# Kernel optimization log

Hardware: AMD Instinct MI355X
Metric: run time of the kernel (lower is better)

## Reference

```python
import jax, jax.numpy as jnp
import numpy as np

B, S, D = 2, 2048, 1024
H, HD = 16, 64


def setup_inputs() -> dict:
    key = jax.random.key(0)
    ks = jax.random.split(key, 10)
    scale = 1.0 / np.sqrt(D)
    inputs_q = jax.random.normal(ks[0], (B, S, D), dtype=jnp.float32)
    inputs_kv = jax.random.normal(ks[1], (B, S, D), dtype=jnp.float32)
    # causal mask, broadcast over batch: True = attend
    mask = jnp.broadcast_to(jnp.tril(jnp.ones((S, S), dtype=bool)), (B, S, S))
    Wq = jax.random.normal(ks[2], (D, H * HD), dtype=jnp.float32) * scale
    bq = jnp.zeros((H * HD,), dtype=jnp.float32)
    Wk = jax.random.normal(ks[3], (D, H * HD), dtype=jnp.float32) * scale
    bk = jnp.zeros((H * HD,), dtype=jnp.float32)
    Wv = jax.random.normal(ks[4], (D, H * HD), dtype=jnp.float32) * scale
    bv = jnp.zeros((H * HD,), dtype=jnp.float32)
    Wo = jax.random.normal(ks[5], (H * HD, D), dtype=jnp.float32) * scale
    bo = jnp.zeros((D,), dtype=jnp.float32)
    return {"inputs_q": inputs_q, "inputs_kv": inputs_kv, "mask": mask,
            "Wq": Wq, "bq": bq, "Wk": Wk, "bk": bk, "Wv": Wv, "bv": bv,
            "Wo": Wo, "bo": bo}


def reference(inputs_q, inputs_kv, mask, Wq, bq, Wk, bk, Wv, bv, Wo, bo):
    b, s_q, _ = inputs_q.shape
    s_k = inputs_kv.shape[1]
    # projections -> [B, S, H, HD]
    q = (inputs_q @ Wq + bq).reshape(b, s_q, H, HD)
    k = (inputs_kv @ Wk + bk).reshape(b, s_k, H, HD)
    v = (inputs_kv @ Wv + bv).reshape(b, s_k, H, HD)
    q = q / jnp.sqrt(jnp.asarray(HD, dtype=q.dtype))
    # scores: [B, H, Sq, Sk]
    attn = jnp.einsum('bqhd,bkhd->bhqk', q, k)
    m = mask[:, None, :, :]  # [B,1,Sq,Sk] broadcast over heads
    attn = jnp.where(m, attn, jnp.asarray(-1e30, dtype=attn.dtype))
    attn = jax.nn.softmax(attn, axis=-1)
    # dropout_rate = 0.0, deterministic -> identity
    out = jnp.einsum('bhqk,bkhd->bqhd', attn, v).reshape(b, s_q, H * HD)
    return out @ Wo + bo
```

## Files before the change

### kernel.cpp

```cpp
#include <hip/hip_runtime.h>

typedef __attribute__((ext_vector_type(4))) float f32x4;
typedef __attribute__((ext_vector_type(8))) short bf16x8;
typedef unsigned short u16;
typedef unsigned int u32;

#define AS1 __attribute__((address_space(1)))
#define AS3 __attribute__((address_space(3)))

#define WAITVM(N) do{ asm volatile("s_waitcnt vmcnt(" #N ")" ::: "memory"); \
                      __builtin_amdgcn_sched_barrier(0); }while(0)
#define RAWBAR    do{ __builtin_amdgcn_s_barrier();                          \
                      __builtin_amdgcn_sched_barrier(0); }while(0)

__device__ __forceinline__ float fast_exp2(float x){
  return __builtin_amdgcn_exp2f(x);
}

__device__ __forceinline__ u16 f2bf(float x){
  u32 u = __float_as_uint(x);
  u += 0x7fffu + ((u >> 16) & 1u);
  return (u16)(u >> 16);
}
__device__ __forceinline__ u16 f2bf_fast(float x){
  return (u16)((__float_as_uint(x) + 0x8000u) >> 16);
}

__global__ __launch_bounds__(256) void prep(const float* __restrict__ W0,
                                            const float* __restrict__ W1,
                                            const float* __restrict__ W2,
                                            const float* __restrict__ W3,
                                            u16* __restrict__ Wt,
                                            const float* __restrict__ inq,
                                            const float* __restrict__ inkv,
                                            u16* __restrict__ Xq,
                                            u16* __restrict__ Xkv)
{
  const int z = blockIdx.z;
  if (z < 4){
    __shared__ float tile[32][33];
    const float* src = z == 0 ? W0 : z == 1 ? W1 : z == 2 ? W2 : W3;
    u16* d = Wt + (size_t)z * 1024 * 1024;
    int tx = threadIdx.x & 31, ty = threadIdx.x >> 5;
    int k0 = blockIdx.x * 32, n0 = blockIdx.y * 32;
    for (int r = 0; r < 4; ++r)
      tile[ty + r * 8][tx] = src[(size_t)(k0 + ty + r * 8) * 1024 + n0 + tx];
    __syncthreads();
    for (int r = 0; r < 4; ++r)
      d[(size_t)(n0 + ty + r * 8) * 1024 + k0 + tx] = f2bf(tile[tx][ty + r * 8]);
  } else {
    const float* src = z == 4 ? inq : inkv;
    u16* dst = z == 4 ? Xq : Xkv;
    int bid = blockIdx.y * 32 + blockIdx.x;
    size_t base4 = ((size_t)bid * 256 + threadIdx.x) * 4;
#pragma unroll
    for (int i = 0; i < 4; ++i){
      float4 v = reinterpret_cast<const float4*>(src)[base4 + i];
      ushort4 o;
      o.x = f2bf(v.x); o.y = f2bf(v.y); o.z = f2bf(v.z); o.w = f2bf(v.w);
      reinterpret_cast<ushort4*>(dst)[base4 + i] = o;
    }
  }
}

__global__ __launch_bounds__(512, 2) void gemm_qkv(const u16* __restrict__ Xq,
                                                   const u16* __restrict__ Xkv,
                                                   const u16* __restrict__ Wt,
                                                   const float* __restrict__ bq,
                                                   const float* __restrict__ bk,
                                                   const float* __restrict__ bv,
                                                   u16* __restrict__ Qb,
                                                   u16* __restrict__ Kb,
                                                   u16* __restrict__ Vt,
                                                   int M, int K)
{
  __shared__ u16 lA[3][256 * 32];
  __shared__ u16 lB[3][256 * 32];
  const int tid = threadIdx.x;
  const int l = tid & 63, w = tid >> 6;
  const int wr = w >> 2, wc = w & 3;
  const int bm0 = blockIdx.x * 256, bn0 = blockIdx.y * 256;
  const int seg = bn0 >> 10;
  const int nloc0 = bn0 & 1023;
  const u16* A = seg ? Xkv : Xq;
  const float* bias = seg == 0 ? bq : seg == 1 ? bk : bv;
  const float scale = seg == 0 ? 0.125f * 1.44269504089f : 1.0f;
  const int lr = l & 15, g4 = l >> 4;

#define STAGE_A(BI, KK) do{                                                   \
  _Pragma("unroll") for (int c_ = 0; c_ < 2; ++c_){                           \
    int e_ = c_ * 512 + tid;                                                  \
    int row_ = e_ >> 2, ch_ = e_ & 3;                                         \
    int sc_ = (ch_ ^ (row_ & 3)) * 8;                                         \
    __builtin_amdgcn_global_load_lds(                                         \
        (const AS1 u32*)(A + (size_t)(bm0 + row_) * K + (KK) * 32 + sc_),     \
        (AS3 u32*)(&lA[BI][e_ * 8]), 16, 0, 0);                               \
  }                                                                           \
}while(0)
#define STAGE_B(BI, KK) do{                                                   \
  _Pragma("unroll") for (int c_ = 0; c_ < 2; ++c_){                           \
    int e_ = c_ * 512 + tid;                                                  \
    int row_ = e_ >> 2, ch_ = e_ & 3;                                         \
    int sc_ = (ch_ ^ (row_ & 3)) * 8;                                         \
    __builtin_amdgcn_global_load_lds(                                         \
        (const AS1 u32*)(Wt + (size_t)(bn0 + row_) * K + (KK) * 32 + sc_),    \
        (AS3 u32*)(&lB[BI][e_ * 8]), 16, 0, 0);                               \
  }                                                                           \
}while(0)

#define RD(LDS, ROW) (*reinterpret_cast<const bf16x8*>(                       \
    reinterpret_cast<const char*>(LDS) + (ROW) * 64 + ((g4 ^ ((ROW) & 3)) << 4)))

  f32x4 acc[8][4];
#pragma unroll
  for (int m = 0; m < 8; ++m)
#pragma unroll
    for (int n = 0; n < 4; ++n) acc[m][n] = (f32x4){0.f, 0.f, 0.f, 0.f};

  STAGE_A(0, 0); STAGE_B(0, 0);
  STAGE_A(1, 1); STAGE_B(1, 1);

#pragma unroll
  for (int k = 0; k < 32; ++k){
    const int cur = k % 3;
    if (k < 30){ STAGE_A((k + 2) % 3, k + 2); WAITVM(6); }
    else if (k == 30){ WAITVM(4); }
    else { WAITVM(0); }
    RAWBAR;

    bf16x8 aLo[4], bF[4];
#pragma unroll
    for (int m = 0; m < 4; ++m)
      aLo[m] = RD(lA[cur], wr * 128 + m * 16 + lr);
#pragma unroll
    for (int n = 0; n < 4; ++n)
      bF[n] = RD(lB[cur], wc * 64 + n * 16 + lr);
    __builtin_amdgcn_s_setprio(1);
#pragma unroll
    for (int m = 0; m < 4; ++m)
#pragma unroll
      for (int n = 0; n < 4; ++n)
        acc[m][n] = __builtin_amdgcn_mfma_f32_16x16x32_bf16(aLo[m], bF[n], acc[m][n], 0, 0, 0);
    __builtin_amdgcn_s_setprio(0);
    RAWBAR;

    if (k < 30) STAGE_B((k + 2) % 3, k + 2);
    bf16x8 aHi[4];
#pragma unroll
    for (int m = 0; m < 4; ++m)
      aHi[m] = RD(lA[cur], wr * 128 + (m + 4) * 16 + lr);
    __builtin_amdgcn_s_setprio(1);
#pragma unroll
    for (int m = 0; m < 4; ++m)
#pragma unroll
      for (int n = 0; n < 4; ++n)
        acc[m + 4][n] = __builtin_amdgcn_mfma_f32_16x16x32_bf16(aHi[m], bF[n], acc[m + 4][n], 0, 0, 0);
    __builtin_amdgcn_s_setprio(0);
    RAWBAR;
  }
#undef STAGE_A
#undef STAGE_B
#undef RD

  const int r0 = g4 * 4;
  if (seg < 2){
    u16* C = seg == 0 ? Qb : Kb;
#pragma unroll
    for (int m = 0; m < 8; ++m)
#pragma unroll
      for (int n = 0; n < 4; ++n){
        int col = nloc0 + wc * 64 + n * 16 + lr;
        float bv_ = bias[col];
#pragma unroll
        for (int r = 0; r < 4; ++r){
          int row = bm0 + wr * 128 + m * 16 + r0 + r;
          C[(size_t)row * 1024 + col] = f2bf((acc[m][n][r] + bv_) * scale);
        }
      }
  } else {
#pragma unroll
    for (int m = 0; m < 8; ++m)
#pragma unroll
      for (int n = 0; n < 4; ++n){
        int col = nloc0 + wc * 64 + n * 16 + lr;
        float bv_ = bias[col];
        int h = col >> 6, hdl = col & 63;
#pragma unroll
        for (int r = 0; r < 4; ++r){
          int row = bm0 + wr * 128 + m * 16 + r0 + r;
          int b = row >> 11, kv = row & 2047;
          size_t off = ((size_t)(b * 16 + h)) * 131072 + (size_t)hdl * 2048 + kv;
          Vt[off] = f2bf(acc[m][n][r] + bv_);
        }
      }
  }
}

__global__ __launch_bounds__(256) void gemm_out(const u16* __restrict__ A,
                                                const u16* __restrict__ Bt,
                                                const float* __restrict__ bias,
                                                float* __restrict__ Cf,
                                                int M, int N, int K)
{
  __shared__ u16 lA[3][64 * 32];
  __shared__ u16 lB[3][128 * 32];
  const int tid = threadIdx.x;
  const int l = tid & 63, w = tid >> 6;
  const int wr = w >> 1, wc = w & 1;
  const int bm0 = blockIdx.x * 64, bn0 = blockIdx.y * 128;
  const int lr = l & 15, lg = (l >> 4) * 8;

#define STAGE_O(BI, KK) do{                                                   \
  {                                                                           \
    int e_ = tid * 8;                                                         \
    int row_ = e_ >> 5, col_ = e_ & 31;                                       \
    __builtin_amdgcn_global_load_lds(                                         \
        (const AS1 u32*)(A + (size_t)(bm0 + row_) * K + (KK) * 32 + col_),    \
        (AS3 u32*)(&lA[BI][e_]), 16, 0, 0);                                   \
  }                                                                           \
  _Pragma("unroll") for (int c_ = 0; c_ < 2; ++c_){                           \
    int e_ = (c_ * 256 + tid) * 8;                                            \
    int row_ = e_ >> 5, col_ = e_ & 31;                                       \
    __builtin_amdgcn_global_load_lds(                                         \
        (const AS1 u32*)(Bt + (size_t)(bn0 + row_) * K + (KK) * 32 + col_),   \
        (AS3 u32*)(&lB[BI][e_]), 16, 0, 0);                                   \
  }                                                                           \
}while(0)

  f32x4 acc[2][4];
#pragma unroll
  for (int m = 0; m < 2; ++m)
#pragma unroll
    for (int n = 0; n < 4; ++n) acc[m][n] = (f32x4){0.f, 0.f, 0.f, 0.f};

  STAGE_O(0, 0);
  STAGE_O(1, 1);

#pragma unroll
  for (int k = 0; k < 32; ++k){
    const int cur = k % 3;
    if (k < 30){ STAGE_O((k + 2) % 3, k + 2); WAITVM(6); }
    else if (k == 30){ WAITVM(3); }
    else { WAITVM(0); }
    RAWBAR;

    bf16x8 aF[2], bF[4];
#pragma unroll
    for (int m = 0; m < 2; ++m)
      aF[m] = *reinterpret_cast<const bf16x8*>(&lA[cur][(wr * 32 + m * 16 + lr) * 32 + lg]);
#pragma unroll
    for (int n = 0; n < 4; ++n)
      bF[n] = *reinterpret_cast<const bf16x8*>(&lB[cur][(wc * 64 + n * 16 + lr) * 32 + lg]);
    __builtin_amdgcn_s_setprio(1);
#pragma unroll
    for (int m = 0; m < 2; ++m)
#pragma unroll
      for (int n = 0; n < 4; ++n)
        acc[m][n] = __builtin_amdgcn_mfma_f32_16x16x32_bf16(aF[m], bF[n], acc[m][n], 0, 0, 0);
    __builtin_amdgcn_s_setprio(0);
    RAWBAR;
  }
#undef STAGE_O

  const int r0 = (l >> 4) * 4;
#pragma unroll
  for (int m = 0; m < 2; ++m)
#pragma unroll
    for (int n = 0; n < 4; ++n){
      int col = bn0 + wc * 64 + n * 16 + lr;
      float bv_ = bias[col];
#pragma unroll
      for (int r = 0; r < 4; ++r){
        int row = bm0 + wr * 32 + m * 16 + r0 + r;
        Cf[(size_t)row * N + col] = acc[m][n][r] + bv_;
      }
    }
}

__global__ __launch_bounds__(512, 2) void attn_fwd(const u16* __restrict__ Qb,
                                                   const u16* __restrict__ Kb,
                                                   const u16* __restrict__ Vt,
                                                   u16* __restrict__ AO, int S)
{
  __shared__ u16 lK[2][64 * 64];
  __shared__ u16 lV[2][64 * 64];
  __shared__ u16 lP[8][16 * 72];
  const int tid = threadIdx.x, l = tid & 63, w = tid >> 6;
  const int j = blockIdx.x;
  const int jj = j & 255;
  const int xcd = jj & 7;
  const int bh = xcd * 4 + ((jj >> 3) & 3);
  const int p = jj >> 5;
  const int qt = (j < 256) ? p : (15 - p);
  const int bb = bh >> 4;
  const size_t baseQK = ((size_t)bb * S) * 1024 + (bh & 15) * 64;
  const u16* gK = Kb + baseQK;
  const u16* gV = Vt + (size_t)bh * 131072;
  const int lr = l & 15, g4 = l >> 4, lg = g4 * 8;

  u16* lPw = (u16*)lP[w];
  bf16x8 ones;
#pragma unroll
  for (int i = 0; i < 8; ++i) ones[i] = (short)0x3F80;

#define STAGE_KV(T, BI) do{                                                   \
  int row_ = tid >> 3, ch_ = tid & 7, sc_ = (ch_ ^ (row_ & 7)) * 8;           \
  __builtin_amdgcn_global_load_lds(                                           \
      (const AS1 u32*)(gK + (size_t)(64 * (T) + row_) * 1024 + sc_),          \
      (AS3 u32*)(&lK[BI][tid * 8]), 16, 0, 0);                                \
  __builtin_amdgcn_global_load_lds(                                           \
      (const AS1 u32*)(gV + (size_t)row_ * 2048 + 64 * (T) + sc_),            \
      (AS3 u32*)(&lV[BI][tid * 8]), 16, 0, 0);                                \
}while(0)

  const int ntb = 2 * qt + 2;
  const int q0 = qt * 128 + w * 16;

  bf16x8 qf[2];
#pragma unroll
  for (int kc = 0; kc < 2; ++kc)
    qf[kc] = *reinterpret_cast<const bf16x8*>(
        Qb + baseQK + (size_t)(q0 + lr) * 1024 + kc * 32 + lg);

  f32x4 acc_o[4], acc_l;
  acc_l = (f32x4){0.f, 0.f, 0.f, 0.f};
#pragma unroll
  for (int n = 0; n < 4; ++n) acc_o[n] = (f32x4){0.f, 0.f, 0.f, 0.f};

  int buf = 0;
  STAGE_KV(0, 0);
  for (int t = 0; t < ntb; ++t){
    if (t + 1 < ntb){ STAGE_KV(t + 1, buf ^ 1); WAITVM(2); }
    else            { WAITVM(0); }
    RAWBAR;

    if (64 * t <= q0 + 15){
      const u16* lKb = lK[buf];
      const u16* lVb = lV[buf];
      f32x4 sA[4];
#pragma unroll
      for (int np = 0; np < 4; ++np) sA[np] = (f32x4){0.f, 0.f, 0.f, 0.f};
      __builtin_amdgcn_s_setprio(1);
#pragma unroll
      for (int kc = 0; kc < 2; ++kc)
#pragma unroll
        for (int np = 0; np < 4; ++np){
          int row = np * 16 + lr, ch = kc * 4 + g4;
          bf16x8 kf = *reinterpret_cast<const bf16x8*>(
              reinterpret_cast<const char*>(lKb) + row * 128 + ((ch ^ (row & 7)) << 4));
          sA[np] = __builtin_amdgcn_mfma_f32_16x16x32_bf16(qf[kc], kf, sA[np], 0, 0, 0);
        }
      __builtin_amdgcn_s_setprio(0);

      const bool needmask = (64 * t + 63 > q0);
      if (needmask){
#pragma unroll
        for (int np = 0; np < 4; ++np){
          int kvg = 64 * t + np * 16 + lr;
#pragma unroll
          for (int r = 0; r < 4; ++r){
            int qg = q0 + g4 * 4 + r;
            float e = fast_exp2(sA[np][r]);
            lPw[(g4 * 4 + r) * 72 + np * 16 + lr] = f2bf_fast((kvg <= qg) ? e : 0.f);
          }
        }
      } else {
#pragma unroll
        for (int np = 0; np < 4; ++np)
#pragma unroll
          for (int r = 0; r < 4; ++r)
            lPw[(g4 * 4 + r) * 72 + np * 16 + lr] = f2bf_fast(fast_exp2(sA[np][r]));
      }

      bf16x8 pf[2];
#pragma unroll
      for (int kc = 0; kc < 2; ++kc)
        pf[kc] = *reinterpret_cast<const bf16x8*>(
            reinterpret_cast<const char*>(lPw) + lr * 144 + (kc * 4 + g4) * 16);
      __builtin_amdgcn_s_setprio(1);
#pragma unroll
      for (int kc = 0; kc < 2; ++kc){
        acc_l = __builtin_amdgcn_mfma_f32_16x16x32_bf16(pf[kc], ones, acc_l, 0, 0, 0);
#pragma unroll
        for (int n = 0; n < 4; ++n){
          int row = n * 16 + lr, ch = kc * 4 + g4;
          bf16x8 vf = *reinterpret_cast<const bf16x8*>(
              reinterpret_cast<const char*>(lVb) + row * 128 + ((ch ^ (row & 7)) << 4));
          acc_o[n] = __builtin_amdgcn_mfma_f32_16x16x32_bf16(pf[kc], vf, acc_o[n], 0, 0, 0);
        }
      }
      __builtin_amdgcn_s_setprio(0);
    }
    RAWBAR;
    buf ^= 1;
  }

  float inv[4];
#pragma unroll
  for (int r = 0; r < 4; ++r) inv[r] = 1.0f / acc_l[r];
#pragma unroll
  for (int n = 0; n < 4; ++n)
#pragma unroll
    for (int r = 0; r < 4; ++r){
      int row = q0 + g4 * 4 + r;
      AO[baseQK + (size_t)row * 1024 + n * 16 + lr] = f2bf(acc_o[n][r] * inv[r]);
    }
#undef STAGE_KV
}

extern "C" void kernel_launch(void* const* d_in, const int* in_sizes, int n_in,
                              void* d_out, int out_size, void* d_ws, size_t ws_size,
                              hipStream_t stream)
{
  const float* inq  = (const float*)d_in[0];
  const float* inkv = (const float*)d_in[1];
  const float* Wq = (const float*)d_in[3];
  const float* bq = (const float*)d_in[4];
  const float* Wk = (const float*)d_in[5];
  const float* bk = (const float*)d_in[6];
  const float* Wv = (const float*)d_in[7];
  const float* bv = (const float*)d_in[8];
  const float* Wo = (const float*)d_in[9];
  const float* bo = (const float*)d_in[10];
  float* out = (float*)d_out;

  const int B = 2, S = 2048, D = 1024;
  const int M = B * S;

  char* ws = (char*)d_ws;
  const size_t MB = 1024ull * 1024ull;
  u16* Xq  = (u16*)(ws + 0 * MB);
  u16* Xkv = (u16*)(ws + 8 * MB);
  u16* Wt  = (u16*)(ws + 16 * MB);
  u16* Wot = (u16*)(ws + 22 * MB);
  u16* Qb  = (u16*)(ws + 24 * MB);
  u16* Kb  = (u16*)(ws + 32 * MB);
  u16* Vtg = (u16*)(ws + 40 * MB);
  u16* AOb = (u16*)(ws + 48 * MB);

  prep<<<dim3(32, 32, 6), 256, 0, stream>>>(Wq, Wk, Wv, Wo, Wt, inq, inkv, Xq, Xkv);

  gemm_qkv<<<dim3(M / 256, 3072 / 256), 512, 0, stream>>>(Xq, Xkv, Wt, bq, bk, bv,
                                                          Qb, Kb, Vtg, M, D);

  attn_fwd<<<dim3(512), 512, 0, stream>>>(Qb, Kb, Vtg, AOb, S);

  gemm_out<<<dim3(M / 64, D / 128), 256, 0, stream>>>(AOb, Wot, bo, out, M, D, D);
}
```

Before: 116.3 us.

## Split causal attention KV range into two halves with separate combine kernel

```diff
diff --git a/kernel.cpp b/kernel.cpp
--- a/kernel.cpp
+++ b/kernel.cpp
@@ -24,6 +24,9 @@
 }
 __device__ __forceinline__ u16 f2bf_fast(float x){
   return (u16)((__float_as_uint(x) + 0x8000u) >> 16);
+}
+__device__ __forceinline__ float bf2f(u16 x){
+  return __uint_as_float((u32)x << 16);
 }
 
 __global__ __launch_bounds__(256) void prep(const float* __restrict__ W0,
@@ -280,7 +283,8 @@
 __global__ __launch_bounds__(512, 2) void attn_fwd(const u16* __restrict__ Qb,
                                                    const u16* __restrict__ Kb,
                                                    const u16* __restrict__ Vt,
-                                                   u16* __restrict__ AO, int S)
+                                                   u16* __restrict__ Po,
+                                                   float* __restrict__ Pl, int S)
 {
   __shared__ u16 lK[2][64 * 64];
   __shared__ u16 lV[2][64 * 64];
@@ -291,7 +295,11 @@
   const int xcd = jj & 7;
   const int bh = xcd * 4 + ((jj >> 3) & 3);
   const int p = jj >> 5;
-  const int qt = (j < 256) ? p : (15 - p);
+  const int rnd = j >> 8;
+  const int qt = (rnd & 1) ? (15 - p) : p;
+  const int half = rnd >> 1;
+  const int t0 = half ? (qt + 1) : 0;
+  const int t1 = (qt + 1) << half ? (half ? (2 * qt + 2) : (qt + 1)) : (qt + 1);
   const int bb = bh >> 4;
   const size_t baseQK = ((size_t)bb * S) * 1024 + (bh & 15) * 64;
   const u16* gK = Kb + baseQK;
@@ -313,7 +321,6 @@
       (AS3 u32*)(&lV[BI][tid * 8]), 16, 0, 0);                                \
 }while(0)
 
-  const int ntb = 2 * qt + 2;
   const int q0 = qt * 128 + w * 16;
 
   bf16x8 qf[2];
@@ -328,10 +335,10 @@
   for (int n = 0; n < 4; ++n) acc_o[n] = (f32x4){0.f, 0.f, 0.f, 0.f};
 
   int buf = 0;
-  STAGE_KV(0, 0);
-  for (int t = 0; t < ntb; ++t){
-    if (t + 1 < ntb){ STAGE_KV(t + 1, buf ^ 1); WAITVM(2); }
-    else            { WAITVM(0); }
+  STAGE_KV(t0, 0);
+  for (int t = t0; t < t1; ++t){
+    if (t + 1 < t1){ STAGE_KV(t + 1, buf ^ 1); WAITVM(2); }
+    else           { WAITVM(0); }
     RAWBAR;
 
     if (64 * t <= q0 + 15){
@@ -395,17 +402,50 @@
     buf ^= 1;
   }
 
-  float inv[4];
-#pragma unroll
-  for (int r = 0; r < 4; ++r) inv[r] = 1.0f / acc_l[r];
+  const int part = (bh * 16 + qt) * 2 + half;
+  u16* po = Po + (size_t)part * 8192;
+  float* pl = Pl + part * 128;
 #pragma unroll
   for (int n = 0; n < 4; ++n)
 #pragma unroll
     for (int r = 0; r < 4; ++r){
-      int row = q0 + g4 * 4 + r;
-      AO[baseQK + (size_t)row * 1024 + n * 16 + lr] = f2bf(acc_o[n][r] * inv[r]);
+      int rl = w * 16 + g4 * 4 + r;
+      po[rl * 64 + n * 16 + lr] = f2bf(acc_o[n][r]);
     }
+  if (lr == 0){
+#pragma unroll
+    for (int r = 0; r < 4; ++r)
+      pl[w * 16 + g4 * 4 + r] = acc_l[r];
+  }
 #undef STAGE_KV
+}
+
+__global__ __launch_bounds__(256) void attn_combine(const u16* __restrict__ Po,
+                                                    const float* __restrict__ Pl,
+                                                    u16* __restrict__ AO, int S)
+{
+  const int g = blockIdx.x;
+  const int bh = g >> 4, qt = g & 15;
+  const int bb = bh >> 4, h = bh & 15;
+  const size_t base = ((size_t)bb * S) * 1024 + h * 64;
+  const u16* o0 = Po + (size_t)(g * 2 + 0) * 8192;
+  const u16* o1 = Po + (size_t)(g * 2 + 1) * 8192;
+  const float* l0 = Pl + (g * 2 + 0) * 128;
+  const float* l1 = Pl + (g * 2 + 1) * 128;
+  const int cg = (threadIdx.x & 15) * 4, rb = threadIdx.x >> 4;
+#pragma unroll
+  for (int r = 0; r < 8; ++r){
+    int row = rb * 8 + r;
+    float inv = 1.0f / (l0[row] + l1[row]);
+    ushort4 a = *reinterpret_cast<const ushort4*>(&o0[row * 64 + cg]);
+    ushort4 b = *reinterpret_cast<const ushort4*>(&o1[row * 64 + cg]);
+    ushort4 o;
+    o.x = f2bf((bf2f(a.x) + bf2f(b.x)) * inv);
+    o.y = f2bf((bf2f(a.y) + bf2f(b.y)) * inv);
+    o.z = f2bf((bf2f(a.z) + bf2f(b.z)) * inv);
+    o.w = f2bf((bf2f(a.w) + bf2f(b.w)) * inv);
+    *reinterpret_cast<ushort4*>(&AO[base + (size_t)(qt * 128 + row) * 1024 + cg]) = o;
+  }
 }
 
 extern "C" void kernel_launch(void* const* d_in, const int* in_sizes, int n_in,
@@ -430,8 +470,10 @@
   char* ws = (char*)d_ws;
   const size_t MB = 1024ull * 1024ull;
   u16* Xq  = (u16*)(ws + 0 * MB);
+  u16* Po  = (u16*)(ws + 0 * MB);
   u16* Xkv = (u16*)(ws + 8 * MB);
   u16* Wt  = (u16*)(ws + 16 * MB);
+  float* Pl = (float*)(ws + 16 * MB);
   u16* Wot = (u16*)(ws + 22 * MB);
   u16* Qb  = (u16*)(ws + 24 * MB);
   u16* Kb  = (u16*)(ws + 32 * MB);
@@ -443,7 +485,9 @@
   gemm_qkv<<<dim3(M / 256, 3072 / 256), 512, 0, stream>>>(Xq, Xkv, Wt, bq, bk, bv,
                                                           Qb, Kb, Vtg, M, D);
 
-  attn_fwd<<<dim3(512), 512, 0, stream>>>(Qb, Kb, Vtg, AOb, S);
+  attn_fwd<<<dim3(1024), 512, 0, stream>>>(Qb, Kb, Vtg, Po, Pl, S);
+
+  attn_combine<<<dim3(512), 256, 0, stream>>>(Po, Pl, AOb, S);
 
   gemm_out<<<dim3(M / 64, D / 128), 256, 0, stream>>>(AOb, Wot, bo, out, M, D, D);
 }
```

Measured after the change: 118.2 us. About the same (+1.7%).

## Restructure QKV GEMM to K=64 double-buffered tiles with half-split LDS layout

Applied to the files above, without the earlier changes.

```diff
diff --git a/kernel.cpp b/kernel.cpp
--- a/kernel.cpp
+++ b/kernel.cpp
@@ -11,6 +11,8 @@
 #define WAITVM(N) do{ asm volatile("s_waitcnt vmcnt(" #N ")" ::: "memory"); \
                       __builtin_amdgcn_sched_barrier(0); }while(0)
 #define RAWBAR    do{ __builtin_amdgcn_s_barrier();                          \
+                      __builtin_amdgcn_sched_barrier(0); }while(0)
+#define LGKM0     do{ asm volatile("s_waitcnt lgkmcnt(0)" ::: "memory");     \
                       __builtin_amdgcn_sched_barrier(0); }while(0)
 
 __device__ __forceinline__ float fast_exp2(float x){
@@ -63,7 +65,7 @@
   }
 }
 
-__global__ __launch_bounds__(512, 2) void gemm_qkv(const u16* __restrict__ Xq,
+__global__ __launch_bounds__(512, 1) void gemm_qkv(const u16* __restrict__ Xq,
                                                    const u16* __restrict__ Xkv,
                                                    const u16* __restrict__ Wt,
                                                    const float* __restrict__ bq,
@@ -74,42 +76,35 @@
                                                    u16* __restrict__ Vt,
                                                    int M, int K)
 {
-  __shared__ u16 lA[3][256 * 32];
-  __shared__ u16 lB[3][256 * 32];
+  __shared__ u16 lA[2][2][128 * 64];
+  __shared__ u16 lB[2][2][128 * 64];
   const int tid = threadIdx.x;
   const int l = tid & 63, w = tid >> 6;
   const int wr = w >> 2, wc = w & 3;
   const int bm0 = blockIdx.x * 256, bn0 = blockIdx.y * 256;
   const int seg = bn0 >> 10;
   const int nloc0 = bn0 & 1023;
-  const u16* A = seg ? Xkv : Xq;
+  const u16* Ag = seg ? Xkv : Xq;
   const float* bias = seg == 0 ? bq : seg == 1 ? bk : bv;
   const float scale = seg == 0 ? 0.125f * 1.44269504089f : 1.0f;
   const int lr = l & 15, g4 = l >> 4;
 
-#define STAGE_A(BI, KK) do{                                                   \
+  const u16* Abase = Ag + (size_t)bm0 * K;
+  const u16* Bbase = Wt + (size_t)bn0 * K;
+
+#define STG(DST, GBASE, H, KT) do{                                            \
   _Pragma("unroll") for (int c_ = 0; c_ < 2; ++c_){                           \
     int e_ = c_ * 512 + tid;                                                  \
-    int row_ = e_ >> 2, ch_ = e_ & 3;                                         \
-    int sc_ = (ch_ ^ (row_ & 3)) * 8;                                         \
+    int row_ = e_ >> 3, ch_ = e_ & 7;                                         \
+    int sc_ = (ch_ ^ (row_ & 7)) * 8;                                         \
     __builtin_amdgcn_global_load_lds(                                         \
-        (const AS1 u32*)(A + (size_t)(bm0 + row_) * K + (KK) * 32 + sc_),     \
-        (AS3 u32*)(&lA[BI][e_ * 8]), 16, 0, 0);                               \
+        (const AS1 u32*)((GBASE) + (size_t)((H) * 128 + row_) * K + (KT) * 64 + sc_), \
+        (AS3 u32*)(&(DST)[e_ * 8]), 16, 0, 0);                                \
   }                                                                           \
 }while(0)
-#define STAGE_B(BI, KK) do{                                                   \
-  _Pragma("unroll") for (int c_ = 0; c_ < 2; ++c_){                           \
-    int e_ = c_ * 512 + tid;                                                  \
-    int row_ = e_ >> 2, ch_ = e_ & 3;                                         \
-    int sc_ = (ch_ ^ (row_ & 3)) * 8;                                         \
-    __builtin_amdgcn_global_load_lds(                                         \
-        (const AS1 u32*)(Wt + (size_t)(bn0 + row_) * K + (KK) * 32 + sc_),    \
-        (AS3 u32*)(&lB[BI][e_ * 8]), 16, 0, 0);                               \
-  }                                                                           \
-}while(0)
-
-#define RD(LDS, ROW) (*reinterpret_cast<const bf16x8*>(                       \
-    reinterpret_cast<const char*>(LDS) + (ROW) * 64 + ((g4 ^ ((ROW) & 3)) << 4)))
+
+#define RDH(PTR, ROW, CH) (*reinterpret_cast<const bf16x8*>(                  \
+    reinterpret_cast<const char*>(PTR) + (ROW) * 128 + ((((CH) ^ ((ROW) & 7))) << 4)))
 
   f32x4 acc[8][4];
 #pragma unroll
@@ -117,50 +112,62 @@
 #pragma unroll
     for (int n = 0; n < 4; ++n) acc[m][n] = (f32x4){0.f, 0.f, 0.f, 0.f};
 
-  STAGE_A(0, 0); STAGE_B(0, 0);
-  STAGE_A(1, 1); STAGE_B(1, 1);
-
-#pragma unroll
-  for (int k = 0; k < 32; ++k){
-    const int cur = k % 3;
-    if (k < 30){ STAGE_A((k + 2) % 3, k + 2); WAITVM(6); }
-    else if (k == 30){ WAITVM(4); }
-    else { WAITVM(0); }
-    RAWBAR;
-
-    bf16x8 aLo[4], bF[4];
-#pragma unroll
-    for (int m = 0; m < 4; ++m)
-      aLo[m] = RD(lA[cur], wr * 128 + m * 16 + lr);
-#pragma unroll
-    for (int n = 0; n < 4; ++n)
-      bF[n] = RD(lB[cur], wc * 64 + n * 16 + lr);
-    __builtin_amdgcn_s_setprio(1);
-#pragma unroll
-    for (int m = 0; m < 4; ++m)
-#pragma unroll
-      for (int n = 0; n < 4; ++n)
-        acc[m][n] = __builtin_amdgcn_mfma_f32_16x16x32_bf16(aLo[m], bF[n], acc[m][n], 0, 0, 0);
-    __builtin_amdgcn_s_setprio(0);
-    RAWBAR;
-
-    if (k < 30) STAGE_B((k + 2) % 3, k + 2);
-    bf16x8 aHi[4];
-#pragma unroll
-    for (int m = 0; m < 4; ++m)
-      aHi[m] = RD(lA[cur], wr * 128 + (m + 4) * 16 + lr);
-    __builtin_amdgcn_s_setprio(1);
-#pragma unroll
-    for (int m = 0; m < 4; ++m)
-#pragma unroll
-      for (int n = 0; n < 4; ++n)
-        acc[m + 4][n] = __builtin_amdgcn_mfma_f32_16x16x32_bf16(aHi[m], bF[n], acc[m + 4][n], 0, 0, 0);
-    __builtin_amdgcn_s_setprio(0);
-    RAWBAR;
+  STG(lA[0][0], Abase, 0, 0); STG(lA[0][1], Abase, 1, 0);
+  STG(lB[0][0], Bbase, 0, 0); STG(lB[0][1], Bbase, 1, 0);
+  WAITVM(0); RAWBAR;
+
+  for (int t = 0; t < 16; ++t){
+    const int d = t & 1, dn = d ^ 1;
+    const u16* la = (const u16*)lA[d][wr];
+    const u16* lb = (const u16*)lB[d][wc >> 1];
+    const int bR0 = (wc & 1) * 64;
+    const bool st = (t < 15);
+
+#pragma unroll
+    for (int kk = 0; kk < 2; ++kk){
+      bf16x8 bF[4];
+      {
+        bf16x8 aF[4];
+#pragma unroll
+        for (int m4 = 0; m4 < 4; ++m4)
+          aF[m4] = RDH(la, m4 * 16 + lr, kk * 4 + g4);
+#pragma unroll
+        for (int n = 0; n < 4; ++n)
+          bF[n] = RDH(lb, bR0 + n * 16 + lr, kk * 4 + g4);
+        if (kk == 0 && st){
+          STG(lA[dn][0], Abase, 0, t + 1); STG(lA[dn][1], Abase, 1, t + 1);
+          STG(lB[dn][0], Bbase, 0, t + 1); STG(lB[dn][1], Bbase, 1, t + 1);
+        }
+        RAWBAR; LGKM0;
+        __builtin_amdgcn_s_setprio(1);
+#pragma unroll
+        for (int m4 = 0; m4 < 4; ++m4)
+#pragma unroll
+          for (int n = 0; n < 4; ++n)
+            acc[m4][n] = __builtin_amdgcn_mfma_f32_16x16x32_bf16(aF[m4], bF[n], acc[m4][n], 0, 0, 0);
+        __builtin_amdgcn_s_setprio(0);
+        RAWBAR;
+      }
+      {
+        bf16x8 aF[4];
+#pragma unroll
+        for (int m4 = 0; m4 < 4; ++m4)
+          aF[m4] = RDH(la, (4 + m4) * 16 + lr, kk * 4 + g4);
+        if (kk == 1) WAITVM(0);
+        RAWBAR; LGKM0;
+        __builtin_amdgcn_s_setprio(1);
+#pragma unroll
+        for (int m4 = 0; m4 < 4; ++m4)
+#pragma unroll
+          for (int n = 0; n < 4; ++n)
+            acc[4 + m4][n] = __builtin_amdgcn_mfma_f32_16x16x32_bf16(aF[m4], bF[n], acc[4 + m4][n], 0, 0, 0);
+        __builtin_amdgcn_s_setprio(0);
+        RAWBAR;
+      }
+    }
   }
-#undef STAGE_A
-#undef STAGE_B
-#undef RD
+#undef STG
+#undef RDH
 
   const int r0 = g4 * 4;
   if (seg < 2){
```

Measured after the change: 117.4 us. Within noise of the previous version (+1.0%).

## Shrink attention tiles to 64 query rows and 32-key blocks with 4-wave blocks

Applied to the files above, without the earlier changes.

```diff
diff --git a/kernel.cpp b/kernel.cpp
--- a/kernel.cpp
+++ b/kernel.cpp
@@ -277,21 +277,22 @@
     }
 }
 
-__global__ __launch_bounds__(512, 2) void attn_fwd(const u16* __restrict__ Qb,
+__global__ __launch_bounds__(256, 4) void attn_fwd(const u16* __restrict__ Qb,
                                                    const u16* __restrict__ Kb,
                                                    const u16* __restrict__ Vt,
                                                    u16* __restrict__ AO, int S)
 {
-  __shared__ u16 lK[2][64 * 64];
-  __shared__ u16 lV[2][64 * 64];
-  __shared__ u16 lP[8][16 * 72];
+  __shared__ u16 lK[2][32 * 64];
+  __shared__ u16 lV[2][64 * 32];
+  __shared__ u16 lP[4][16 * 36];
   const int tid = threadIdx.x, l = tid & 63, w = tid >> 6;
   const int j = blockIdx.x;
   const int jj = j & 255;
+  const int rnd = j >> 8;
   const int xcd = jj & 7;
   const int bh = xcd * 4 + ((jj >> 3) & 3);
   const int p = jj >> 5;
-  const int qt = (j < 256) ? p : (15 - p);
+  const int i = (rnd < 2) ? (p * 2 + rnd) : (31 - p * 2 - (rnd - 2));
   const int bb = bh >> 4;
   const size_t baseQK = ((size_t)bb * S) * 1024 + (bh & 15) * 64;
   const u16* gK = Kb + baseQK;
@@ -301,20 +302,21 @@
   u16* lPw = (u16*)lP[w];
   bf16x8 ones;
 #pragma unroll
-  for (int i = 0; i < 8; ++i) ones[i] = (short)0x3F80;
+  for (int q = 0; q < 8; ++q) ones[q] = (short)0x3F80;
 
 #define STAGE_KV(T, BI) do{                                                   \
-  int row_ = tid >> 3, ch_ = tid & 7, sc_ = (ch_ ^ (row_ & 7)) * 8;           \
+  int rk_ = tid >> 3, ck_ = tid & 7, sk_ = (ck_ ^ (rk_ & 7)) * 8;             \
   __builtin_amdgcn_global_load_lds(                                           \
-      (const AS1 u32*)(gK + (size_t)(64 * (T) + row_) * 1024 + sc_),          \
+      (const AS1 u32*)(gK + (size_t)(32 * (T) + rk_) * 1024 + sk_),           \
       (AS3 u32*)(&lK[BI][tid * 8]), 16, 0, 0);                                \
+  int rv_ = tid >> 2, cv_ = tid & 3, sv_ = (cv_ ^ (rv_ & 3)) * 8;             \
   __builtin_amdgcn_global_load_lds(                                           \
-      (const AS1 u32*)(gV + (size_t)row_ * 2048 + 64 * (T) + sc_),            \
+      (const AS1 u32*)(gV + (size_t)rv_ * 2048 + 32 * (T) + sv_),             \
       (AS3 u32*)(&lV[BI][tid * 8]), 16, 0, 0);                                \
 }while(0)
 
-  const int ntb = 2 * qt + 2;
-  const int q0 = qt * 128 + w * 16;
+  const int ntb = 2 * i + 2;
+  const int q0 = i * 64 + w * 16;
 
   bf16x8 qf[2];
 #pragma unroll
@@ -334,17 +336,17 @@
     else            { WAITVM(0); }
     RAWBAR;
 
-    if (64 * t <= q0 + 15){
+    if (32 * t <= q0 + 15){
       const u16* lKb = lK[buf];
       const u16* lVb = lV[buf];
-      f32x4 sA[4];
-#pragma unroll
-      for (int np = 0; np < 4; ++np) sA[np] = (f32x4){0.f, 0.f, 0.f, 0.f};
+      f32x4 sA[2];
+#pragma unroll
+      for (int np = 0; np < 2; ++np) sA[np] = (f32x4){0.f, 0.f, 0.f, 0.f};
       __builtin_amdgcn_s_setprio(1);
 #pragma unroll
       for (int kc = 0; kc < 2; ++kc)
 #pragma unroll
-        for (int np = 0; np < 4; ++np){
+        for (int np = 0; np < 2; ++np){
           int row = np * 16 + lr, ch = kc * 4 + g4;
           bf16x8 kf = *reinterpret_cast<const bf16x8*>(
               reinterpret_cast<const char*>(lKb) + row * 128 + ((ch ^ (row & 7)) << 4));
@@ -352,42 +354,36 @@
         }
       __builtin_amdgcn_s_setprio(0);
 
-      const bool needmask = (64 * t + 63 > q0);
+      const bool needmask = (32 * t + 31 > q0);
       if (needmask){
 #pragma unroll
-        for (int np = 0; np < 4; ++np){
-          int kvg = 64 * t + np * 16 + lr;
+        for (int np = 0; np < 2; ++np){
+          int kvg = 32 * t + np * 16 + lr;
 #pragma unroll
           for (int r = 0; r < 4; ++r){
             int qg = q0 + g4 * 4 + r;
             float e = fast_exp2(sA[np][r]);
-            lPw[(g4 * 4 + r) * 72 + np * 16 + lr] = f2bf_fast((kvg <= qg) ? e : 0.f);
+            lPw[(g4 * 4 + r) * 36 + np * 16 + lr] = f2bf_fast((kvg <= qg) ? e : 0.f);
           }
         }
       } else {
 #pragma unroll
-        for (int np = 0; np < 4; ++np)
+        for (int np = 0; np < 2; ++np)
 #pragma unroll
           for (int r = 0; r < 4; ++r)
-            lPw[(g4 * 4 + r) * 72 + np * 16 + lr] = f2bf_fast(fast_exp2(sA[np][r]));
+            lPw[(g4 * 4 + r) * 36 + np * 16 + lr] = f2bf_fast(fast_exp2(sA[np][r]));
       }
 
-      bf16x8 pf[2];
-#pragma unroll
-      for (int kc = 0; kc < 2; ++kc)
-        pf[kc] = *reinterpret_cast<const bf16x8*>(
-            reinterpret_cast<const char*>(lPw) + lr * 144 + (kc * 4 + g4) * 16);
+      bf16x8 pf = *reinterpret_cast<const bf16x8*>(
+          reinterpret_cast<const char*>(lPw) + lr * 72 + g4 * 16);
       __builtin_amdgcn_s_setprio(1);
-#pragma unroll
-      for (int kc = 0; kc < 2; ++kc){
-        acc_l = __builtin_amdgcn_mfma_f32_16x16x32_bf16(pf[kc], ones, acc_l, 0, 0, 0);
-#pragma unroll
-        for (int n = 0; n < 4; ++n){
-          int row = n * 16 + lr, ch = kc * 4 + g4;
-          bf16x8 vf = *reinterpret_cast<const bf16x8*>(
-              reinterpret_cast<const char*>(lVb) + row * 128 + ((ch ^ (row & 7)) << 4));
-          acc_o[n] = __builtin_amdgcn_mfma_f32_16x16x32_bf16(pf[kc], vf, acc_o[n], 0, 0, 0);
-        }
+      acc_l = __builtin_amdgcn_mfma_f32_16x16x32_bf16(pf, ones, acc_l, 0, 0, 0);
+#pragma unroll
+      for (int n = 0; n < 4; ++n){
+        int row = n * 16 + lr;
+        bf16x8 vf = *reinterpret_cast<const bf16x8*>(
+            reinterpret_cast<const char*>(lVb) + row * 64 + ((g4 ^ (row & 3)) << 4));
+        acc_o[n] = __builtin_amdgcn_mfma_f32_16x16x32_bf16(pf, vf, acc_o[n], 0, 0, 0);
       }
       __builtin_amdgcn_s_setprio(0);
     }
@@ -443,7 +439,7 @@
   gemm_qkv<<<dim3(M / 256, 3072 / 256), 512, 0, stream>>>(Xq, Xkv, Wt, bq, bk, bv,
                                                           Qb, Kb, Vtg, M, D);
 
-  attn_fwd<<<dim3(512), 512, 0, stream>>>(Qb, Kb, Vtg, AOb, S);
+  attn_fwd<<<dim3(1024), 256, 0, stream>>>(Qb, Kb, Vtg, AOb, S);
 
   gemm_out<<<dim3(M / 64, D / 128), 256, 0, stream>>>(AOb, Wot, bo, out, M, D, D);
 }
```

After: 134.0 us. +15.2%, slower.
